# Optimization experiments

Measured on AMD Instinct MI355X. Metric: run time of the kernel, lower is better.

The kernel has to match this reference:

```python
import jax, jax.numpy as jnp
import numpy as np

NEG = -1.0e9

def setup_inputs() -> dict:
    key = jax.random.key(0)
    ks = jax.random.split(key, 8)
    B, H, S, D = 4, 8, 1024, 64
    Q = jax.random.normal(ks[0], (B, H, S, D), dtype=jnp.float32)
    K = jax.random.normal(ks[1], (B, H, S, D), dtype=jnp.float32)
    V = jax.random.normal(ks[2], (B, H, S, D), dtype=jnp.float32)
    attn_mask_col = jax.random.randint(ks[3], (B, H, S, S), 0, 2).astype(jnp.bool_)
    adj_matrix = jax.random.uniform(ks[4], (B, H, S, S), dtype=jnp.float32)
    dist_matrix = jax.random.uniform(ks[5], (B, H, S, S), dtype=jnp.float32)
    conv_w = jax.random.normal(ks[6], (3,), dtype=jnp.float32)
    conv_b = jax.random.normal(ks[7], (1,), dtype=jnp.float32)
    return {"Q": Q, "K": K, "V": V, "attn_mask_col": attn_mask_col,
            "adj_matrix": adj_matrix, "dist_matrix": dist_matrix,
            "conv_w": conv_w, "conv_b": conv_b}

def reference(Q, K, V, attn_mask_col, adj_matrix, dist_matrix, conv_w, conv_b):
    d_k = Q.shape[-1]
    # scores: [B,H,Sq,Sk]
    scores = jnp.einsum('bhqd,bhkd->bhqk', Q, K) / jnp.sqrt(jnp.float32(d_k))
    scores = jnp.where(attn_mask_col, NEG, scores)
    scores = jax.nn.softmax(scores, axis=-1)
    # 1x1 Conv2d(3->1) over stacked [scores, dist, adj] == learned weighted sum
    weighted = conv_w[0] * scores + conv_w[1] * dist_matrix + conv_w[2] * adj_matrix + conv_b[0]
    weighted = jnp.where(attn_mask_col, NEG, weighted)
    attn = jax.nn.softmax(weighted, axis=-1)  # dropout p=0 -> identity
    context = jnp.einsum('bhqk,bhkd->bhqd', attn, V)
    return (context, attn)
```

## Files before the change

kernel.cpp:

```cpp
#include <hip/hip_runtime.h>

typedef _Float16 f16;
typedef _Float16 f16x8 __attribute__((ext_vector_type(8)));
typedef _Float16 f16x4 __attribute__((ext_vector_type(4)));
typedef float f32x4 __attribute__((ext_vector_type(4)));
typedef int   i32x4 __attribute__((ext_vector_type(4)));

constexpr int B_ = 4, H_ = 8, S_ = 1024, D_ = 64;
constexpr int BQ = 32;
constexpr int NT = 512;
constexpr int KC = 128;
constexpr int QH_LD = 72;
constexpr int SC_LD = 1032;
constexpr float LOG2E = 1.44269504f;

__device__ __forceinline__ float wred(float v) {
#pragma unroll
  for (int off = 32; off > 0; off >>= 1) v += __shfl_xor(v, off);
  return v;
}

__global__ __launch_bounds__(NT)
void fused_attn(const float* __restrict__ Q, const float* __restrict__ K,
                const float* __restrict__ V, const int* __restrict__ mask,
                const float* __restrict__ adj, const float* __restrict__ dist,
                const float* __restrict__ cw, const float* __restrict__ cb,
                float* __restrict__ outC, float* __restrict__ outA)
{
  __shared__ __align__(16) f16 Qh[BQ * QH_LD];
  __shared__ __align__(16) f16 sch[BQ * SC_LD];
  __shared__ float rs1w[8][BQ];
  __shared__ float rinv2[BQ];

  const int tid = threadIdx.x;
  const int sw = (blockIdx.x & 7) * 128 + (blockIdx.x >> 3);
  const int qt = sw & 31;
  const int bh = sw >> 5;
  const int q0 = qt * BQ;
  const int wv = tid >> 6;
  const int ln = tid & 63;
  const int lg = ln >> 4;
  const int li = ln & 15;

  const float* Qp = Q + ((size_t)bh * S_ + q0) * D_;
  const float* Kp = K + (size_t)bh * S_ * D_;
  const float* Vp = V + (size_t)bh * S_ * D_;
  const size_t rb = ((size_t)bh * S_ + q0) * S_;

  {
    const int q = tid >> 4, c4 = (tid & 15) << 2;
    float4 v = *(const float4*)(Qp + q * D_ + c4);
    f16* d = &Qh[q * QH_LD + c4];
    d[0] = (f16)v.x; d[1] = (f16)v.y; d[2] = (f16)v.z; d[3] = (f16)v.w;
  }
  const float w0 = cw[0], w1 = cw[1], w2 = cw[2], bb = cb[0];
  __syncthreads();

  f16x8 aq00 = *(const f16x8*)&Qh[li * QH_LD + 0 * 32 + lg * 8];
  f16x8 aq01 = *(const f16x8*)&Qh[li * QH_LD + 1 * 32 + lg * 8];
  f16x8 aq10 = *(const f16x8*)&Qh[(16 + li) * QH_LD + 0 * 32 + lg * 8];
  f16x8 aq11 = *(const f16x8*)&Qh[(16 + li) * QH_LD + 1 * 32 + lg * 8];

  const int n0 = wv * 16;
  float rs0[4] = {0.f, 0.f, 0.f, 0.f};
  float rs1[4] = {0.f, 0.f, 0.f, 0.f};
#pragma unroll 2
  for (int c = 0; c < 8; ++c) {
    const int kg = c * KC + n0 + li;
    const float* Kr = Kp + (size_t)kg * D_ + lg * 8;
    const float4 ka = *(const float4*)(Kr + 0);
    const float4 kb = *(const float4*)(Kr + 4);
    const float4 kc2 = *(const float4*)(Kr + 32);
    const float4 kd = *(const float4*)(Kr + 36);
    f16x8 b0, b1;
    b0[0] = (f16)ka.x; b0[1] = (f16)ka.y; b0[2] = (f16)ka.z; b0[3] = (f16)ka.w;
    b0[4] = (f16)kb.x; b0[5] = (f16)kb.y; b0[6] = (f16)kb.z; b0[7] = (f16)kb.w;
    b1[0] = (f16)kc2.x; b1[1] = (f16)kc2.y; b1[2] = (f16)kc2.z; b1[3] = (f16)kc2.w;
    b1[4] = (f16)kd.x; b1[5] = (f16)kd.y; b1[6] = (f16)kd.z; b1[7] = (f16)kd.w;
    f32x4 acc0 = {0.f, 0.f, 0.f, 0.f};
    f32x4 acc1 = {0.f, 0.f, 0.f, 0.f};
    acc0 = __builtin_amdgcn_mfma_f32_16x16x32_f16(aq00, b0, acc0, 0, 0, 0);
    acc1 = __builtin_amdgcn_mfma_f32_16x16x32_f16(aq10, b0, acc1, 0, 0, 0);
    acc0 = __builtin_amdgcn_mfma_f32_16x16x32_f16(aq01, b1, acc0, 0, 0, 0);
    acc1 = __builtin_amdgcn_mfma_f32_16x16x32_f16(aq11, b1, acc1, 0, 0, 0);
#pragma unroll
    for (int r = 0; r < 4; ++r) {
      const int m = lg * 4 + r;
      const f16 e0 = (f16)exp2f(acc0[r] * (0.125f * LOG2E));
      const f16 e1 = (f16)exp2f(acc1[r] * (0.125f * LOG2E));
      sch[m * SC_LD + kg] = e0;
      sch[(16 + m) * SC_LD + kg] = e1;
      rs0[r] += (float)e0;
      rs1[r] += (float)e1;
    }
  }
#pragma unroll
  for (int r = 0; r < 4; ++r) {
    rs0[r] += __shfl_xor(rs0[r], 1); rs0[r] += __shfl_xor(rs0[r], 2);
    rs0[r] += __shfl_xor(rs0[r], 4); rs0[r] += __shfl_xor(rs0[r], 8);
    rs1[r] += __shfl_xor(rs1[r], 1); rs1[r] += __shfl_xor(rs1[r], 2);
    rs1[r] += __shfl_xor(rs1[r], 4); rs1[r] += __shfl_xor(rs1[r], 8);
  }
  if (li == 0) {
#pragma unroll
    for (int r = 0; r < 4; ++r) {
      rs1w[wv][lg * 4 + r] = rs0[r];
      rs1w[wv][16 + lg * 4 + r] = rs1[r];
    }
  }
  __syncthreads();

#pragma unroll
  for (int rr = 0; rr < 4; ++rr) {
    const int q = 4 * wv + rr;
    const size_t base = rb + (size_t)q * S_;
    const int k0 = ln * 4;
    const i32x4 mv0 = __builtin_nontemporal_load((const i32x4*)(mask + base + k0 + 0));
    const i32x4 mv1 = __builtin_nontemporal_load((const i32x4*)(mask + base + k0 + 256));
    const i32x4 mv2 = __builtin_nontemporal_load((const i32x4*)(mask + base + k0 + 512));
    const i32x4 mv3 = __builtin_nontemporal_load((const i32x4*)(mask + base + k0 + 768));
    const f32x4 dv0 = __builtin_nontemporal_load((const f32x4*)(dist + base + k0 + 0));
    const f32x4 dv1 = __builtin_nontemporal_load((const f32x4*)(dist + base + k0 + 256));
    const f32x4 dv2 = __builtin_nontemporal_load((const f32x4*)(dist + base + k0 + 512));
    const f32x4 dv3 = __builtin_nontemporal_load((const f32x4*)(dist + base + k0 + 768));
    const f32x4 av0 = __builtin_nontemporal_load((const f32x4*)(adj + base + k0 + 0));
    const f32x4 av1 = __builtin_nontemporal_load((const f32x4*)(adj + base + k0 + 256));
    const f32x4 av2 = __builtin_nontemporal_load((const f32x4*)(adj + base + k0 + 512));
    const f32x4 av3 = __builtin_nontemporal_load((const f32x4*)(adj + base + k0 + 768));
    const f16x4 ef0 = *(const f16x4*)&sch[q * SC_LD + k0 + 0];
    const f16x4 ef1 = *(const f16x4*)&sch[q * SC_LD + k0 + 256];
    const f16x4 ef2 = *(const f16x4*)&sch[q * SC_LD + k0 + 512];
    const f16x4 ef3 = *(const f16x4*)&sch[q * SC_LD + k0 + 768];
    __builtin_amdgcn_sched_barrier(0);
    float corr =
        (mv0[0] ? (float)ef0[0] : 0.f) + (mv0[1] ? (float)ef0[1] : 0.f) +
        (mv0[2] ? (float)ef0[2] : 0.f) + (mv0[3] ? (float)ef0[3] : 0.f) +
        (mv1[0] ? (float)ef1[0] : 0.f) + (mv1[1] ? (float)ef1[1] : 0.f) +
        (mv1[2] ? (float)ef1[2] : 0.f) + (mv1[3] ? (float)ef1[3] : 0.f) +
        (mv2[0] ? (float)ef2[0] : 0.f) + (mv2[1] ? (float)ef2[1] : 0.f) +
        (mv2[2] ? (float)ef2[2] : 0.f) + (mv2[3] ? (float)ef2[3] : 0.f) +
        (mv3[0] ? (float)ef3[0] : 0.f) + (mv3[1] ? (float)ef3[1] : 0.f) +
        (mv3[2] ? (float)ef3[2] : 0.f) + (mv3[3] ? (float)ef3[3] : 0.f);
    float tq = 0.f;
#pragma unroll
    for (int w = 0; w < 8; ++w) tq += rs1w[w][q];
    corr = wred(corr);
    const float i1 = 1.f / (tq - corr);
    const float W0 = w0 * i1 * LOG2E, W1 = w1 * LOG2E, W2 = w2 * LOG2E;
    const float BBL = bb * LOG2E;
    f16x4 af0, af1, af2, af3;
    float s2 = 0.f;
#define CSM(AF, MV, DV, AV, EF)                                               \
    {                                                                         \
      const float t0 = fmaf(W0, (float)EF[0], fmaf(W1, DV[0], fmaf(W2, AV[0], BBL))); \
      const float t1 = fmaf(W0, (float)EF[1], fmaf(W1, DV[1], fmaf(W2, AV[1], BBL))); \
      const float t2 = fmaf(W0, (float)EF[2], fmaf(W1, DV[2], fmaf(W2, AV[2], BBL))); \
      const float t3 = fmaf(W0, (float)EF[3], fmaf(W1, DV[3], fmaf(W2, AV[3], BBL))); \
      const float a0 = MV[0] ? 0.f : exp2f(t0);                               \
      const float a1 = MV[1] ? 0.f : exp2f(t1);                               \
      const float a2 = MV[2] ? 0.f : exp2f(t2);                               \
      const float a3 = MV[3] ? 0.f : exp2f(t3);                               \
      AF[0] = (f16)a0; AF[1] = (f16)a1; AF[2] = (f16)a2; AF[3] = (f16)a3;     \
      s2 += a0 + a1 + a2 + a3;                                                \
    }
    CSM(af0, mv0, dv0, av0, ef0)
    CSM(af1, mv1, dv1, av1, ef1)
    CSM(af2, mv2, dv2, av2, ef2)
    CSM(af3, mv3, dv3, av3, ef3)
#undef CSM
    *(f16x4*)&sch[q * SC_LD + k0 + 0]   = af0;
    *(f16x4*)&sch[q * SC_LD + k0 + 256] = af1;
    *(f16x4*)&sch[q * SC_LD + k0 + 512] = af2;
    *(f16x4*)&sch[q * SC_LD + k0 + 768] = af3;
    s2 = wred(s2);
    const float i2 = 1.f / s2;
    if (ln == 0) rinv2[q] = i2;
    f32x4 o;
    o[0] = (float)af0[0] * i2; o[1] = (float)af0[1] * i2;
    o[2] = (float)af0[2] * i2; o[3] = (float)af0[3] * i2;
    __builtin_nontemporal_store(o, (f32x4*)(outA + base + k0 + 0));
    o[0] = (float)af1[0] * i2; o[1] = (float)af1[1] * i2;
    o[2] = (float)af1[2] * i2; o[3] = (float)af1[3] * i2;
    __builtin_nontemporal_store(o, (f32x4*)(outA + base + k0 + 256));
    o[0] = (float)af2[0] * i2; o[1] = (float)af2[1] * i2;
    o[2] = (float)af2[2] * i2; o[3] = (float)af2[3] * i2;
    __builtin_nontemporal_store(o, (f32x4*)(outA + base + k0 + 512));
    o[0] = (float)af3[0] * i2; o[1] = (float)af3[1] * i2;
    o[2] = (float)af3[2] * i2; o[3] = (float)af3[3] * i2;
    __builtin_nontemporal_store(o, (f32x4*)(outA + base + k0 + 768));
  }
  __syncthreads();

  const int dt = wv & 3;
  const int kh = wv >> 2;
  const int d0 = dt * 16 + li;
  f32x4 c0 = {0.f, 0.f, 0.f, 0.f};
  f32x4 c1 = {0.f, 0.f, 0.f, 0.f};
#pragma unroll 2
  for (int c = 0; c < 4; ++c) {
#pragma unroll
    for (int s = 0; s < 4; ++s) {
      const int kbase = kh * 512 + c * 128 + s * 32;
      const float* Vc = Vp + (size_t)(kbase + lg * 8) * D_ + d0;
      f16x8 bfr;
#pragma unroll
      for (int j = 0; j < 8; ++j) bfr[j] = (f16)Vc[(size_t)j * D_];
      f16x8 a0 = *(const f16x8*)&sch[li * SC_LD + kbase + lg * 8];
      f16x8 a1 = *(const f16x8*)&sch[(16 + li) * SC_LD + kbase + lg * 8];
      c0 = __builtin_amdgcn_mfma_f32_16x16x32_f16(a0, bfr, c0, 0, 0, 0);
      c1 = __builtin_amdgcn_mfma_f32_16x16x32_f16(a1, bfr, c1, 0, 0, 0);
    }
  }
  __syncthreads();
  float* fscr = reinterpret_cast<float*>(sch);
  *(f32x4*)&fscr[(wv * 64 + ln) * 8 + 0] = c0;
  *(f32x4*)&fscr[(wv * 64 + ln) * 8 + 4] = c1;
  __syncthreads();
  if (tid < 256) {
    const int t = tid >> 6, l2 = tid & 63;
    const int g2 = l2 >> 4, n = l2 & 15;
#pragma unroll
    for (int g = 0; g < 2; ++g) {
      f32x4 p  = *(const f32x4*)&fscr[((t) * 64 + l2) * 8 + 4 * g];
      f32x4 p2 = *(const f32x4*)&fscr[((t + 4) * 64 + l2) * 8 + 4 * g];
#pragma unroll
      for (int r = 0; r < 4; ++r) {
        const int m = g * 16 + g2 * 4 + r;
        outC[((size_t)bh * S_ + q0 + m) * D_ + t * 16 + n] =
            (p[r] + p2[r]) * rinv2[m];
      }
    }
  }
}

extern "C" void kernel_launch(void* const* d_in, const int* in_sizes, int n_in,
                              void* d_out, int out_size, void* d_ws, size_t ws_size,
                              hipStream_t stream) {
  const float* Q    = (const float*)d_in[0];
  const float* K    = (const float*)d_in[1];
  const float* V    = (const float*)d_in[2];
  const int*   mask = (const int*)  d_in[3];
  const float* adj  = (const float*)d_in[4];
  const float* dist = (const float*)d_in[5];
  const float* cw   = (const float*)d_in[6];
  const float* cb   = (const float*)d_in[7];

  float* outC = (float*)d_out;
  float* outA = outC + (size_t)B_ * H_ * S_ * D_;

  fused_attn<<<dim3(B_ * H_ * (S_ / BQ)), NT, 0, stream>>>(
      Q, K, V, mask, adj, dist, cw, cb, outC, outA);
}
```

Before: 125.8 us.

## Double query tile to 64 rows per block to halve K/V re-reads

```diff
diff --git a/kernel.cpp b/kernel.cpp
--- a/kernel.cpp
+++ b/kernel.cpp
@@ -7,9 +7,8 @@
 typedef int   i32x4 __attribute__((ext_vector_type(4)));
 
 constexpr int B_ = 4, H_ = 8, S_ = 1024, D_ = 64;
-constexpr int BQ = 32;
+constexpr int BQ = 64;
 constexpr int NT = 512;
-constexpr int KC = 128;
 constexpr int QH_LD = 72;
 constexpr int SC_LD = 1032;
 constexpr float LOG2E = 1.44269504f;
@@ -19,6 +18,10 @@
   for (int off = 32; off > 0; off >>= 1) v += __shfl_xor(v, off);
   return v;
 }
+
+#define PACK8(DST, X0, X1)                                                    \
+  DST[0] = (f16)X0.x; DST[1] = (f16)X0.y; DST[2] = (f16)X0.z; DST[3] = (f16)X0.w; \
+  DST[4] = (f16)X1.x; DST[5] = (f16)X1.y; DST[6] = (f16)X1.z; DST[7] = (f16)X1.w;
 
 __global__ __launch_bounds__(NT)
 void fused_attn(const float* __restrict__ Q, const float* __restrict__ K,
@@ -33,9 +36,9 @@
   __shared__ float rinv2[BQ];
 
   const int tid = threadIdx.x;
-  const int sw = (blockIdx.x & 7) * 128 + (blockIdx.x >> 3);
-  const int qt = sw & 31;
-  const int bh = sw >> 5;
+  const int sw = (blockIdx.x & 7) * 64 + (blockIdx.x >> 3);
+  const int qt = sw & 15;
+  const int bh = sw >> 4;
   const int q0 = qt * BQ;
   const int wv = tid >> 6;
   const int ln = tid & 63;
@@ -47,8 +50,10 @@
   const float* Vp = V + (size_t)bh * S_ * D_;
   const size_t rb = ((size_t)bh * S_ + q0) * S_;
 
-  {
-    const int q = tid >> 4, c4 = (tid & 15) << 2;
+#pragma unroll
+  for (int i = 0; i < 2; ++i) {
+    const int f = tid + NT * i;
+    const int q = f >> 4, c4 = (f & 15) << 2;
     float4 v = *(const float4*)(Qp + q * D_ + c4);
     f16* d = &Qh[q * QH_LD + c4];
     d[0] = (f16)v.x; d[1] = (f16)v.y; d[2] = (f16)v.z; d[3] = (f16)v.w;
@@ -56,42 +61,58 @@
   const float w0 = cw[0], w1 = cw[1], w2 = cw[2], bb = cb[0];
   __syncthreads();
 
-  f16x8 aq00 = *(const f16x8*)&Qh[li * QH_LD + 0 * 32 + lg * 8];
-  f16x8 aq01 = *(const f16x8*)&Qh[li * QH_LD + 1 * 32 + lg * 8];
-  f16x8 aq10 = *(const f16x8*)&Qh[(16 + li) * QH_LD + 0 * 32 + lg * 8];
-  f16x8 aq11 = *(const f16x8*)&Qh[(16 + li) * QH_LD + 1 * 32 + lg * 8];
+  f16x8 aq00 = *(const f16x8*)&Qh[(0  + li) * QH_LD + 0 + lg * 8];
+  f16x8 aq01 = *(const f16x8*)&Qh[(0  + li) * QH_LD + 32 + lg * 8];
+  f16x8 aq10 = *(const f16x8*)&Qh[(16 + li) * QH_LD + 0 + lg * 8];
+  f16x8 aq11 = *(const f16x8*)&Qh[(16 + li) * QH_LD + 32 + lg * 8];
+  f16x8 aq20 = *(const f16x8*)&Qh[(32 + li) * QH_LD + 0 + lg * 8];
+  f16x8 aq21 = *(const f16x8*)&Qh[(32 + li) * QH_LD + 32 + lg * 8];
+  f16x8 aq30 = *(const f16x8*)&Qh[(48 + li) * QH_LD + 0 + lg * 8];
+  f16x8 aq31 = *(const f16x8*)&Qh[(48 + li) * QH_LD + 32 + lg * 8];
 
   const int n0 = wv * 16;
   float rs0[4] = {0.f, 0.f, 0.f, 0.f};
   float rs1[4] = {0.f, 0.f, 0.f, 0.f};
+  float rs2[4] = {0.f, 0.f, 0.f, 0.f};
+  float rs3[4] = {0.f, 0.f, 0.f, 0.f};
 #pragma unroll 2
   for (int c = 0; c < 8; ++c) {
-    const int kg = c * KC + n0 + li;
+    const int kg = c * 128 + n0 + li;
     const float* Kr = Kp + (size_t)kg * D_ + lg * 8;
     const float4 ka = *(const float4*)(Kr + 0);
     const float4 kb = *(const float4*)(Kr + 4);
     const float4 kc2 = *(const float4*)(Kr + 32);
     const float4 kd = *(const float4*)(Kr + 36);
     f16x8 b0, b1;
-    b0[0] = (f16)ka.x; b0[1] = (f16)ka.y; b0[2] = (f16)ka.z; b0[3] = (f16)ka.w;
-    b0[4] = (f16)kb.x; b0[5] = (f16)kb.y; b0[6] = (f16)kb.z; b0[7] = (f16)kb.w;
-    b1[0] = (f16)kc2.x; b1[1] = (f16)kc2.y; b1[2] = (f16)kc2.z; b1[3] = (f16)kc2.w;
-    b1[4] = (f16)kd.x; b1[5] = (f16)kd.y; b1[6] = (f16)kd.z; b1[7] = (f16)kd.w;
-    f32x4 acc0 = {0.f, 0.f, 0.f, 0.f};
-    f32x4 acc1 = {0.f, 0.f, 0.f, 0.f};
-    acc0 = __builtin_amdgcn_mfma_f32_16x16x32_f16(aq00, b0, acc0, 0, 0, 0);
-    acc1 = __builtin_amdgcn_mfma_f32_16x16x32_f16(aq10, b0, acc1, 0, 0, 0);
-    acc0 = __builtin_amdgcn_mfma_f32_16x16x32_f16(aq01, b1, acc0, 0, 0, 0);
-    acc1 = __builtin_amdgcn_mfma_f32_16x16x32_f16(aq11, b1, acc1, 0, 0, 0);
+    PACK8(b0, ka, kb)
+    PACK8(b1, kc2, kd)
+    f32x4 a0 = {0.f, 0.f, 0.f, 0.f};
+    f32x4 a1 = {0.f, 0.f, 0.f, 0.f};
+    f32x4 a2 = {0.f, 0.f, 0.f, 0.f};
+    f32x4 a3 = {0.f, 0.f, 0.f, 0.f};
+    a0 = __builtin_amdgcn_mfma_f32_16x16x32_f16(aq00, b0, a0, 0, 0, 0);
+    a1 = __builtin_amdgcn_mfma_f32_16x16x32_f16(aq10, b0, a1, 0, 0, 0);
+    a2 = __builtin_amdgcn_mfma_f32_16x16x32_f16(aq20, b0, a2, 0, 0, 0);
+    a3 = __builtin_amdgcn_mfma_f32_16x16x32_f16(aq30, b0, a3, 0, 0, 0);
+    a0 = __builtin_amdgcn_mfma_f32_16x16x32_f16(aq01, b1, a0, 0, 0, 0);
+    a1 = __builtin_amdgcn_mfma_f32_16x16x32_f16(aq11, b1, a1, 0, 0, 0);
+    a2 = __builtin_amdgcn_mfma_f32_16x16x32_f16(aq21, b1, a2, 0, 0, 0);
+    a3 = __builtin_amdgcn_mfma_f32_16x16x32_f16(aq31, b1, a3, 0, 0, 0);
 #pragma unroll
     for (int r = 0; r < 4; ++r) {
       const int m = lg * 4 + r;
-      const f16 e0 = (f16)exp2f(acc0[r] * (0.125f * LOG2E));
-      const f16 e1 = (f16)exp2f(acc1[r] * (0.125f * LOG2E));
-      sch[m * SC_LD + kg] = e0;
+      const f16 e0 = (f16)exp2f(a0[r] * (0.125f * LOG2E));
+      const f16 e1 = (f16)exp2f(a1[r] * (0.125f * LOG2E));
+      const f16 e2 = (f16)exp2f(a2[r] * (0.125f * LOG2E));
+      const f16 e3 = (f16)exp2f(a3[r] * (0.125f * LOG2E));
+      sch[(0  + m) * SC_LD + kg] = e0;
       sch[(16 + m) * SC_LD + kg] = e1;
+      sch[(32 + m) * SC_LD + kg] = e2;
+      sch[(48 + m) * SC_LD + kg] = e3;
       rs0[r] += (float)e0;
       rs1[r] += (float)e1;
+      rs2[r] += (float)e2;
+      rs3[r] += (float)e3;
     }
   }
 #pragma unroll
@@ -100,19 +121,25 @@
     rs0[r] += __shfl_xor(rs0[r], 4); rs0[r] += __shfl_xor(rs0[r], 8);
     rs1[r] += __shfl_xor(rs1[r], 1); rs1[r] += __shfl_xor(rs1[r], 2);
     rs1[r] += __shfl_xor(rs1[r], 4); rs1[r] += __shfl_xor(rs1[r], 8);
+    rs2[r] += __shfl_xor(rs2[r], 1); rs2[r] += __shfl_xor(rs2[r], 2);
+    rs2[r] += __shfl_xor(rs2[r], 4); rs2[r] += __shfl_xor(rs2[r], 8);
+    rs3[r] += __shfl_xor(rs3[r], 1); rs3[r] += __shfl_xor(rs3[r], 2);
+    rs3[r] += __shfl_xor(rs3[r], 4); rs3[r] += __shfl_xor(rs3[r], 8);
   }
   if (li == 0) {
 #pragma unroll
     for (int r = 0; r < 4; ++r) {
-      rs1w[wv][lg * 4 + r] = rs0[r];
+      rs1w[wv][0  + lg * 4 + r] = rs0[r];
       rs1w[wv][16 + lg * 4 + r] = rs1[r];
-    }
-  }
-  __syncthreads();
-
-#pragma unroll
-  for (int rr = 0; rr < 4; ++rr) {
-    const int q = 4 * wv + rr;
+      rs1w[wv][32 + lg * 4 + r] = rs2[r];
+      rs1w[wv][48 + lg * 4 + r] = rs3[r];
+    }
+  }
+  __syncthreads();
+
+#pragma unroll
+  for (int rr = 0; rr < 8; ++rr) {
+    const int q = 8 * wv + rr;
     const size_t base = rb + (size_t)q * S_;
     const int k0 = ln * 4;
     const i32x4 mv0 = __builtin_nontemporal_load((const i32x4*)(mask + base + k0 + 0));
@@ -196,33 +223,41 @@
   const int d0 = dt * 16 + li;
   f32x4 c0 = {0.f, 0.f, 0.f, 0.f};
   f32x4 c1 = {0.f, 0.f, 0.f, 0.f};
+  f32x4 c2 = {0.f, 0.f, 0.f, 0.f};
+  f32x4 c3 = {0.f, 0.f, 0.f, 0.f};
 #pragma unroll 2
-  for (int c = 0; c < 4; ++c) {
-#pragma unroll
-    for (int s = 0; s < 4; ++s) {
-      const int kbase = kh * 512 + c * 128 + s * 32;
-      const float* Vc = Vp + (size_t)(kbase + lg * 8) * D_ + d0;
-      f16x8 bfr;
-#pragma unroll
-      for (int j = 0; j < 8; ++j) bfr[j] = (f16)Vc[(size_t)j * D_];
-      f16x8 a0 = *(const f16x8*)&sch[li * SC_LD + kbase + lg * 8];
-      f16x8 a1 = *(const f16x8*)&sch[(16 + li) * SC_LD + kbase + lg * 8];
-      c0 = __builtin_amdgcn_mfma_f32_16x16x32_f16(a0, bfr, c0, 0, 0, 0);
-      c1 = __builtin_amdgcn_mfma_f32_16x16x32_f16(a1, bfr, c1, 0, 0, 0);
-    }
+  for (int t = 0; t < 16; ++t) {
+    const int kb = kh * 512 + t * 32;
+    const float* Vc = Vp + (size_t)(kb + lg * 8) * D_ + d0;
+    f16x8 bfr;
+#pragma unroll
+    for (int j = 0; j < 8; ++j) bfr[j] = (f16)Vc[(size_t)j * D_];
+    f16x8 p0 = *(const f16x8*)&sch[(0  + li) * SC_LD + kb + lg * 8];
+    f16x8 p1 = *(const f16x8*)&sch[(16 + li) * SC_LD + kb + lg * 8];
+    f16x8 p2 = *(const f16x8*)&sch[(32 + li) * SC_LD + kb + lg * 8];
+    f16x8 p3 = *(const f16x8*)&sch[(48 + li) * SC_LD + kb + lg * 8];
+    c0 = __builtin_amdgcn_mfma_f32_16x16x32_f16(p0, bfr, c0, 0, 0, 0);
+    c1 = __builtin_amdgcn_mfma_f32_16x16x32_f16(p1, bfr, c1, 0, 0, 0);
+    c2 = __builtin_amdgcn_mfma_f32_16x16x32_f16(p2, bfr, c2, 0, 0, 0);
+    c3 = __builtin_amdgcn_mfma_f32_16x16x32_f16(p3, bfr, c3, 0, 0, 0);
   }
   __syncthreads();
   float* fscr = reinterpret_cast<float*>(sch);
-  *(f32x4*)&fscr[(wv * 64 + ln) * 8 + 0] = c0;
-  *(f32x4*)&fscr[(wv * 64 + ln) * 8 + 4] = c1;
+  {
+    float* p = &fscr[(wv * 64 + ln) * 16];
+    *(f32x4*)(p + 0)  = c0;
+    *(f32x4*)(p + 4)  = c1;
+    *(f32x4*)(p + 8)  = c2;
+    *(f32x4*)(p + 12) = c3;
+  }
   __syncthreads();
   if (tid < 256) {
     const int t = tid >> 6, l2 = tid & 63;
     const int g2 = l2 >> 4, n = l2 & 15;
 #pragma unroll
-    for (int g = 0; g < 2; ++g) {
-      f32x4 p  = *(const f32x4*)&fscr[((t) * 64 + l2) * 8 + 4 * g];
-      f32x4 p2 = *(const f32x4*)&fscr[((t + 4) * 64 + l2) * 8 + 4 * g];
+    for (int g = 0; g < 4; ++g) {
+      f32x4 p  = *(const f32x4*)&fscr[((t) * 64 + l2) * 16 + 4 * g];
+      f32x4 p2 = *(const f32x4*)&fscr[((t + 4) * 64 + l2) * 16 + 4 * g];
 #pragma unroll
       for (int r = 0; r < 4; ++r) {
         const int m = g * 16 + g2 * 4 + r;
```

Result: no change. 127.4 us (+1.3%).
